# Optimization experiments

Measured on AMD Instinct MI355X. Metric: run time of the kernel, lower is better.

Reference implementation:

```python
import jax, jax.numpy as jnp
import numpy as np

EPS = 1e-08

def setup_inputs() -> dict:
    key = jax.random.key(0)
    x = jax.random.normal(key, (8192,), dtype=jnp.float32)
    return {"x": x}

def reference(x):
    xf = x.reshape(-1)
    n = xf.shape[0]
    min_x = jnp.min(xf)
    # shift so all values are non-negative only when min is negative (matches torch branch)
    xf = jnp.where(min_x < 0, xf - min_x, xf)
    mu = jnp.mean(xf) + EPS
    # explicit O(n^2) pairwise abs-diff sum, same math as the torch module
    sum_diff = jnp.sum(jnp.abs(xf[None, :] - xf[:, None]))
    gini = sum_diff / (2.0 * (n * n) * mu)
    return gini
```

## Files before the change

### kernel.cpp

```cpp
#include <hip/hip_runtime.h>


#define EPS 1e-8f

__global__ void __launch_bounds__(256) gini_pair_partial(
    const float* __restrict__ x, float* __restrict__ partials, int n) {
    __shared__ __align__(16) float sm[8192];
    const int nchunks = n >> 2;
    {
        const float4* xv = (const float4*)x;
        float4* smv = (float4*)sm;
        for (int i = threadIdx.x; i < nchunks; i += 256) smv[i] = xv[i];
    }
    __syncthreads();

    const int ngroups = n >> 3;
    const int gA = blockIdx.x;
    const int gB = ngroups - 1 - gA;
    const int t  = threadIdx.x;

    float rA[8], rB[8];
    #pragma unroll
    for (int i = 0; i < 8; ++i) {
        rA[i] = sm[gA * 8 + i];
        rB[i] = sm[gB * 8 + i];
    }

    float acc[8];
    #pragma unroll
    for (int i = 0; i < 8; ++i) acc[i] = 0.0f;

    const float4* sm4 = (const float4*)sm;

    for (int c = 2 * gA + t; c < nchunks; c += 256) {
        float4 v = sm4[c];
        #pragma unroll
        for (int i = 0; i < 8; ++i)
            acc[i] += (fabsf(rA[i] - v.x) + fabsf(rA[i] - v.y)) +
                      (fabsf(rA[i] - v.z) + fabsf(rA[i] - v.w));
    }
    for (int c = 2 * gB + t; c < nchunks; c += 256) {
        float4 v = sm4[c];
        #pragma unroll
        for (int i = 0; i < 8; ++i)
            acc[i] += (fabsf(rB[i] - v.x) + fabsf(rB[i] - v.y)) +
                      (fabsf(rB[i] - v.z) + fabsf(rB[i] - v.w));
    }

    float a = ((acc[0] + acc[1]) + (acc[2] + acc[3])) +
              ((acc[4] + acc[5]) + (acc[6] + acc[7]));

    if (t == 0) {
        float s = 0.0f;
        #pragma unroll
        for (int i = 0; i < 8; ++i)
            #pragma unroll
            for (int j = i + 1; j < 8; ++j) s += fabsf(rA[i] - rA[j]);
        a -= s;
    }
    if (t == 1) {
        float s = 0.0f;
        #pragma unroll
        for (int i = 0; i < 8; ++i)
            #pragma unroll
            for (int j = i + 1; j < 8; ++j) s += fabsf(rB[i] - rB[j]);
        a -= s;
    }

    float lmin = 3.4e38f, lsum = 0.0f;
    if (blockIdx.x == 0) {
        for (int i = t; i < n; i += 256) {
            float v = sm[i];
            lmin = fminf(lmin, v);
            lsum += v;
        }
    }

    #pragma unroll
    for (int off = 32; off > 0; off >>= 1) {
        a += __shfl_down(a, off, 64);
        if (blockIdx.x == 0) {
            lmin = fminf(lmin, __shfl_down(lmin, off, 64));
            lsum += __shfl_down(lsum, off, 64);
        }
    }
    __shared__ float wsum[4], wmin[4], wssum[4];
    int wave = threadIdx.x >> 6;
    if ((threadIdx.x & 63) == 0) {
        wsum[wave] = a;
        wmin[wave] = lmin;
        wssum[wave] = lsum;
    }
    __syncthreads();
    if (threadIdx.x == 0) {
        partials[blockIdx.x] = (wsum[0] + wsum[1]) + (wsum[2] + wsum[3]);
        if (blockIdx.x == 0) {
            partials[gridDim.x]     = fminf(fminf(wmin[0], wmin[1]),
                                            fminf(wmin[2], wmin[3]));
            partials[gridDim.x + 1] = (wssum[0] + wssum[1]) +
                                      (wssum[2] + wssum[3]);
        }
    }
}

__global__ void __launch_bounds__(256) gini_finalize(
    const float* __restrict__ partials, int nblocks,
    float* __restrict__ out, int n) {
    float psum = 0.0f;
    for (int i = threadIdx.x; i < nblocks; i += 256) psum += partials[i];

    #pragma unroll
    for (int off = 32; off > 0; off >>= 1) psum += __shfl_down(psum, off, 64);
    __shared__ float spsum[4];
    int wave = threadIdx.x >> 6;
    if ((threadIdx.x & 63) == 0) spsum[wave] = psum;
    __syncthreads();
    if (threadIdx.x == 0) {
        float mn  = partials[nblocks];
        float sum = partials[nblocks + 1];
        float sd  = 2.0f * ((spsum[0] + spsum[1]) + (spsum[2] + spsum[3]));
        float shifted_sum = (mn < 0.0f) ? (sum - (float)n * mn) : sum;
        float mu = shifted_sum / (float)n + EPS;
        out[0] = sd / (2.0f * (float)n * (float)n * mu);
    }
}

extern "C" void kernel_launch(void* const* d_in, const int* in_sizes, int n_in,
                              void* d_out, int out_size, void* d_ws, size_t ws_size,
                              hipStream_t stream) {
    const float* x = (const float*)d_in[0];
    float* out = (float*)d_out;
    float* partials = (float*)d_ws;
    int n = in_sizes[0];

    int ngroups = n >> 3;
    int nblocks = ngroups >> 1;
    gini_pair_partial<<<nblocks, 256, 0, stream>>>(x, partials, n);
    gini_finalize<<<1, 256, 0, stream>>>(partials, nblocks, out, n);
}
```

Measured before the change: 59.32 us.

## Halve grid to four row-groups per 512-thread block and distribute min/sum

Each block now handles four 8-row groups with 512 threads instead of two with 256, so half as many blocks each reload the full 32 KB input into shared memory. The global min and sum are computed per block from the groups it already holds in registers and reduced in the finalize kernel, so block 0 no longer scans the whole array serially. Finalize shrinks to a single wave. In exchange, fewer blocks (256) may leave some compute units lightly loaded, and each thread runs four inner loops.

```diff
diff --git a/kernel.cpp b/kernel.cpp
--- a/kernel.cpp
+++ b/kernel.cpp
@@ -3,27 +3,33 @@
 
 #define EPS 1e-8f
 
-__global__ void __launch_bounds__(256) gini_pair_partial(
+__global__ void __launch_bounds__(512) gini_pair_partial(
     const float* __restrict__ x, float* __restrict__ partials, int n) {
     __shared__ __align__(16) float sm[8192];
     const int nchunks = n >> 2;
     {
         const float4* xv = (const float4*)x;
         float4* smv = (float4*)sm;
-        for (int i = threadIdx.x; i < nchunks; i += 256) smv[i] = xv[i];
+        for (int i = threadIdx.x; i < nchunks; i += 512) smv[i] = xv[i];
     }
     __syncthreads();
 
     const int ngroups = n >> 3;
-    const int gA = blockIdx.x;
-    const int gB = ngroups - 1 - gA;
+    const int nb = gridDim.x;
+    const int b  = blockIdx.x;
+    const int g0 = b;
+    const int g1 = ngroups - 1 - b;
+    const int g2 = nb + b;
+    const int g3 = ngroups - 1 - nb - b;
     const int t  = threadIdx.x;
 
-    float rA[8], rB[8];
+    float r0[8], r1[8], r2[8], r3[8];
     #pragma unroll
     for (int i = 0; i < 8; ++i) {
-        rA[i] = sm[gA * 8 + i];
-        rB[i] = sm[gB * 8 + i];
+        r0[i] = sm[g0 * 8 + i];
+        r1[i] = sm[g1 * 8 + i];
+        r2[i] = sm[g2 * 8 + i];
+        r3[i] = sm[g3 * 8 + i];
     }
 
     float acc[8];
@@ -32,19 +38,33 @@
 
     const float4* sm4 = (const float4*)sm;
 
-    for (int c = 2 * gA + t; c < nchunks; c += 256) {
+    for (int c = 2 * g0 + t; c < nchunks; c += 512) {
         float4 v = sm4[c];
         #pragma unroll
         for (int i = 0; i < 8; ++i)
-            acc[i] += (fabsf(rA[i] - v.x) + fabsf(rA[i] - v.y)) +
-                      (fabsf(rA[i] - v.z) + fabsf(rA[i] - v.w));
+            acc[i] += (fabsf(r0[i] - v.x) + fabsf(r0[i] - v.y)) +
+                      (fabsf(r0[i] - v.z) + fabsf(r0[i] - v.w));
     }
-    for (int c = 2 * gB + t; c < nchunks; c += 256) {
+    for (int c = 2 * g1 + t; c < nchunks; c += 512) {
         float4 v = sm4[c];
         #pragma unroll
         for (int i = 0; i < 8; ++i)
-            acc[i] += (fabsf(rB[i] - v.x) + fabsf(rB[i] - v.y)) +
-                      (fabsf(rB[i] - v.z) + fabsf(rB[i] - v.w));
+            acc[i] += (fabsf(r1[i] - v.x) + fabsf(r1[i] - v.y)) +
+                      (fabsf(r1[i] - v.z) + fabsf(r1[i] - v.w));
+    }
+    for (int c = 2 * g2 + t; c < nchunks; c += 512) {
+        float4 v = sm4[c];
+        #pragma unroll
+        for (int i = 0; i < 8; ++i)
+            acc[i] += (fabsf(r2[i] - v.x) + fabsf(r2[i] - v.y)) +
+                      (fabsf(r2[i] - v.z) + fabsf(r2[i] - v.w));
+    }
+    for (int c = 2 * g3 + t; c < nchunks; c += 512) {
+        float4 v = sm4[c];
+        #pragma unroll
+        for (int i = 0; i < 8; ++i)
+            acc[i] += (fabsf(r3[i] - v.x) + fabsf(r3[i] - v.y)) +
+                      (fabsf(r3[i] - v.z) + fabsf(r3[i] - v.w));
     }
 
     float a = ((acc[0] + acc[1]) + (acc[2] + acc[3])) +
@@ -55,7 +75,7 @@
         #pragma unroll
         for (int i = 0; i < 8; ++i)
             #pragma unroll
-            for (int j = i + 1; j < 8; ++j) s += fabsf(rA[i] - rA[j]);
+            for (int j = i + 1; j < 8; ++j) s += fabsf(r0[i] - r0[j]);
         a -= s;
     }
     if (t == 1) {
@@ -63,63 +83,67 @@
         #pragma unroll
         for (int i = 0; i < 8; ++i)
             #pragma unroll
-            for (int j = i + 1; j < 8; ++j) s += fabsf(rB[i] - rB[j]);
+            for (int j = i + 1; j < 8; ++j) s += fabsf(r1[i] - r1[j]);
+        a -= s;
+    }
+    if (t == 2) {
+        float s = 0.0f;
+        #pragma unroll
+        for (int i = 0; i < 8; ++i)
+            #pragma unroll
+            for (int j = i + 1; j < 8; ++j) s += fabsf(r2[i] - r2[j]);
+        a -= s;
+    }
+    if (t == 3) {
+        float s = 0.0f;
+        #pragma unroll
+        for (int i = 0; i < 8; ++i)
+            #pragma unroll
+            for (int j = i + 1; j < 8; ++j) s += fabsf(r3[i] - r3[j]);
         a -= s;
     }
 
-    float lmin = 3.4e38f, lsum = 0.0f;
-    if (blockIdx.x == 0) {
-        for (int i = t; i < n; i += 256) {
-            float v = sm[i];
-            lmin = fminf(lmin, v);
-            lsum += v;
-        }
+    float mn = r0[0];
+    float sum = 0.0f;
+    #pragma unroll
+    for (int i = 0; i < 8; ++i) {
+        mn = fminf(fminf(mn, fminf(r0[i], r1[i])), fminf(r2[i], r3[i]));
+        sum += (r0[i] + r1[i]) + (r2[i] + r3[i]);
     }
 
     #pragma unroll
-    for (int off = 32; off > 0; off >>= 1) {
-        a += __shfl_down(a, off, 64);
-        if (blockIdx.x == 0) {
-            lmin = fminf(lmin, __shfl_down(lmin, off, 64));
-            lsum += __shfl_down(lsum, off, 64);
-        }
-    }
-    __shared__ float wsum[4], wmin[4], wssum[4];
-    int wave = threadIdx.x >> 6;
-    if ((threadIdx.x & 63) == 0) {
-        wsum[wave] = a;
-        wmin[wave] = lmin;
-        wssum[wave] = lsum;
-    }
+    for (int off = 32; off > 0; off >>= 1) a += __shfl_down(a, off, 64);
+
+    __shared__ float wsum[8];
+    if ((t & 63) == 0) wsum[t >> 6] = a;
     __syncthreads();
-    if (threadIdx.x == 0) {
-        partials[blockIdx.x] = (wsum[0] + wsum[1]) + (wsum[2] + wsum[3]);
-        if (blockIdx.x == 0) {
-            partials[gridDim.x]     = fminf(fminf(wmin[0], wmin[1]),
-                                            fminf(wmin[2], wmin[3]));
-            partials[gridDim.x + 1] = (wssum[0] + wssum[1]) +
-                                      (wssum[2] + wssum[3]);
-        }
+    if (t == 0) {
+        float tot = ((wsum[0] + wsum[1]) + (wsum[2] + wsum[3])) +
+                    ((wsum[4] + wsum[5]) + (wsum[6] + wsum[7]));
+        partials[b]          = tot;
+        partials[nb + b]     = mn;
+        partials[2 * nb + b] = sum;
     }
 }
 
-__global__ void __launch_bounds__(256) gini_finalize(
+__global__ void __launch_bounds__(64) gini_finalize(
     const float* __restrict__ partials, int nblocks,
     float* __restrict__ out, int n) {
-    float psum = 0.0f;
-    for (int i = threadIdx.x; i < nblocks; i += 256) psum += partials[i];
-
+    float psum = 0.0f, pmn = 3.4e38f, ps = 0.0f;
+    for (int i = threadIdx.x; i < nblocks; i += 64) {
+        psum += partials[i];
+        pmn = fminf(pmn, partials[nblocks + i]);
+        ps  += partials[2 * nblocks + i];
+    }
     #pragma unroll
-    for (int off = 32; off > 0; off >>= 1) psum += __shfl_down(psum, off, 64);
-    __shared__ float spsum[4];
-    int wave = threadIdx.x >> 6;
-    if ((threadIdx.x & 63) == 0) spsum[wave] = psum;
-    __syncthreads();
+    for (int off = 32; off > 0; off >>= 1) {
+        psum += __shfl_down(psum, off, 64);
+        pmn = fminf(pmn, __shfl_down(pmn, off, 64));
+        ps  += __shfl_down(ps, off, 64);
+    }
     if (threadIdx.x == 0) {
-        float mn  = partials[nblocks];
-        float sum = partials[nblocks + 1];
-        float sd  = 2.0f * ((spsum[0] + spsum[1]) + (spsum[2] + spsum[3]));
-        float shifted_sum = (mn < 0.0f) ? (sum - (float)n * mn) : sum;
+        float sd = 2.0f * psum;
+        float shifted_sum = (pmn < 0.0f) ? (ps - (float)n * pmn) : ps;
         float mu = shifted_sum / (float)n + EPS;
         out[0] = sd / (2.0f * (float)n * (float)n * mu);
     }
@@ -134,7 +158,7 @@
     int n = in_sizes[0];
 
     int ngroups = n >> 3;
-    int nblocks = ngroups >> 1;
-    gini_pair_partial<<<nblocks, 256, 0, stream>>>(x, partials, n);
-    gini_finalize<<<1, 256, 0, stream>>>(partials, nblocks, out, n);
+    int nblocks = ngroups >> 2;
+    gini_pair_partial<<<nblocks, 512, 0, stream>>>(x, partials, n);
+    gini_finalize<<<1, 64, 0, stream>>>(partials, nblocks, out, n);
 }
```

Result: no change. 58.64 us (-1.1%).
